# Kernel optimization log

Hardware: AMD Instinct MI355X
Metric: run time of the kernel (lower is better)

The kernel has to match this reference:

```python
import jax, jax.numpy as jnp
import numpy as np

B, N, D, R, W, H, I = 256, 2048, 128, 4, 1, 1024, 1024
CI = I + R * D                       # controller input size (1536)
IF = 2 * D * W + 2 * W + 1 + 4 * R + D * R   # interface size (787)
OPI = H + R * D                      # output_proj input (1536)


def _norm(v):
    # F.normalize(dim=-1): x / max(||x||, eps)
    return v / jnp.maximum(jnp.linalg.norm(v, axis=-1, keepdims=True), 1e-12)


def setup_inputs() -> dict:
    key = jax.random.key(0)
    ks = jax.random.split(key, 16)
    u = lambda k, shape, fan: jax.random.uniform(k, shape, jnp.float32, -1.0 / np.sqrt(fan), 1.0 / np.sqrt(fan))
    return {
        "x": jax.random.normal(ks[0], (B, I), jnp.float32),
        "memory": jax.random.normal(ks[1], (N, D), jnp.float32) * np.sqrt(2.0 / (N + D)),  # xavier-ish
        "usage": jax.random.uniform(ks[2], (N,), jnp.float32),          # usage in [0,1)
        "link": jax.random.normal(ks[3], (N, N), jnp.float32) * 0.01,   # non-trivial link state
        "W_ih": u(ks[4], (4 * H, CI), H),
        "W_hh": u(ks[5], (4 * H, H), H),
        "b_ih": u(ks[6], (4 * H,), H),
        "b_hh": u(ks[7], (4 * H,), H),
        "W_if": u(ks[8], (IF, H), H),
        "b_if": u(ks[9], (IF,), H),
        "W_out": u(ks[10], (H, OPI), OPI),
        "b_out": u(ks[11], (H,), OPI),
    }


def reference(x, memory, usage, link, W_ih, W_hh, b_ih, b_hh, W_if, b_if, W_out, b_out):
    # initial uniform read weights (prev state at first step)
    prev_rw = jnp.full((B, R, N), 1.0 / N, x.dtype)
    read_flat = (prev_rw @ memory).reshape(B, -1)                 # (B, R*D)
    cin = jnp.concatenate([x, read_flat], axis=-1)                # (B, CI)

    # single LSTM step, h0 = c0 = 0, torch gate order i,f,g,o
    g = cin @ W_ih.T + b_ih + b_hh
    gi, gf, gg, go = jnp.split(g, 4, axis=-1)
    c = jax.nn.sigmoid(gi) * jnp.tanh(gg)
    h = jax.nn.sigmoid(go) * jnp.tanh(c)                          # (B, H) controller out

    itf = h @ W_if.T + b_if                                       # (B, IF)
    o = 0
    write_vals = itf[:, o:o + D * W].reshape(B, W, D); o += D * W
    erase = jax.nn.sigmoid(itf[:, o:o + D * W]).reshape(B, W, D); o += D * W
    write_gates = jax.nn.sigmoid(itf[:, o:o + W]); o += W         # (B, W)
    alloc_gate = jax.nn.sigmoid(itf[:, o:o + 1]); o += 1          # (B, 1)
    o += W                                                        # free gates (parsed, unused)
    read_modes = jax.nn.softmax(itf[:, o:o + 3 * R].reshape(B, R, 3), -1); o += 3 * R
    read_str = jax.nn.softplus(itf[:, o:o + R]); o += R           # (B, R)
    read_keys = itf[:, o:o + D * R].reshape(B, R, D)

    # content addressing for the write (strength = 1)
    mem_n = _norm(memory)
    cw = jax.nn.softmax(_norm(write_vals.mean(1)) @ mem_n.T, -1)  # (B, N)

    # allocation weighting: sorted-usage cumprod (per source semantics)
    idx = jnp.argsort(usage)
    su = usage[idx]
    cp = jnp.cumprod(1.0 - su)
    alloc_s = jnp.concatenate([su[:1], su[1:] * cp[:-1]])
    alloc = jnp.zeros_like(usage).at[idx].set(alloc_s)[None, :] * alloc_gate  # (B, N)

    write_w = write_gates[:, :, None] * (0.5 * cw + 0.5 * alloc)[:, None, :]  # (B, W, N)

    # temporal link update: batch-mean of diag-masked outer product, decay 0.9
    lu = jnp.einsum('bwn,bwm->nm', write_w, write_w) / B
    lu = lu * (1.0 - jnp.eye(N, dtype=lu.dtype))
    link_new = link * 0.9 + lu * 0.1

    # memory write (erase then add, batch-mean)
    ev = erase * write_gates[:, :, None]
    av = write_vals * write_gates[:, :, None]
    erase_mat = jnp.einsum('bwn,bwd->nd', write_w, ev) / B
    add_mat = jnp.einsum('bwn,bwd->nd', write_w, av) / B
    mem_new = memory * (1.0 - erase_mat) + add_mat

    # read addressing on updated memory and updated link (all R heads vectorized)
    sim = jnp.einsum('brd,nd->brn', _norm(read_keys), _norm(mem_new))
    content_r = jax.nn.softmax(sim * read_str[:, :, None], -1)    # (B, R, N)
    backward_w = jnp.einsum('brn,nm->brm', prev_rw, link_new)     # mode 1: prev @ L
    forward_w = jnp.einsum('brn,mn->brm', prev_rw, link_new)      # mode 2: prev @ L^T
    new_rw = (read_modes[..., 0:1] * content_r
              + read_modes[..., 1:2] * backward_w
              + read_modes[..., 2:3] * forward_w)                 # (B, R, N)

    read_out = (new_rw @ mem_new).reshape(B, -1)                  # (B, R*D)
    out = jnp.concatenate([h, read_out], axis=-1) @ W_out.T + b_out
    return out
```

## Files before the change

### kernel.cpp

```cpp
#include <hip/hip_runtime.h>
#include <cmath>

#define DEVI __device__ __forceinline__

DEVI float sigm(float x){ return 1.f/(1.f+expf(-x)); }

typedef __attribute__((ext_vector_type(8))) _Float16 half8;
typedef __attribute__((ext_vector_type(4))) _Float16 half4;
typedef __attribute__((ext_vector_type(4))) float float4v;


__global__ void k_zero(float* __restrict__ p, int n){
  int i = blockIdx.x*256 + threadIdx.x;
  if (i < n) p[i] = 0.f;
}

__global__ __launch_bounds__(256) void k_stage1(
    const float* __restrict__ mem, float* __restrict__ cm, _Float16* __restrict__ mem_h,
    const float* __restrict__ usage, float* __restrict__ alloc,
    const float* __restrict__ link, float* __restrict__ rsl, float* __restrict__ cslp)
{
  __shared__ float smem[4][132];
  const int blk = blockIdx.x, t = threadIdx.x;
  const int wv = t >> 6, lane = t & 63;

  if (blk < 128){
    int rbase = blk*16 + wv*4;
    float x0[4], x1[4], ss[4];
    #pragma unroll
    for (int u = 0; u < 4; u++){
      const float* a = mem + (size_t)(rbase+u)*128;
      x0[u] = a[lane]; x1[u] = a[lane+64];
    }
    #pragma unroll
    for (int u = 0; u < 4; u++) ss[u] = x0[u]*x0[u] + x1[u]*x1[u];
    #pragma unroll
    for (int o = 1; o < 64; o <<= 1){
      #pragma unroll
      for (int u = 0; u < 4; u++) ss[u] += __shfl_xor(ss[u], o);
    }
    float c0 = 0.f, c1 = 0.f;
    #pragma unroll
    for (int u = 0; u < 4; u++){
      float invn = 1.f / fmaxf(sqrtf(ss[u]), 1e-12f);
      mem_h[(size_t)(rbase+u)*128 + lane]      = (_Float16)(x0[u]*invn);
      mem_h[(size_t)(rbase+u)*128 + 64 + lane] = (_Float16)(x1[u]*invn);
      c0 += x0[u]; c1 += x1[u];
    }
    smem[wv][lane] = c0; smem[wv][64+lane] = c1;
    __syncthreads();
    if (t < 128) atomicAdd(&cm[t], smem[0][t]+smem[1][t]+smem[2][t]+smem[3][t]);
  } else if (blk < 384){
    int pb = blk - 128;
    int r0 = pb*8;
    int c0 = t*8;
    float4v v0[8], v1[8];
    #pragma unroll
    for (int u = 0; u < 8; u++){
      const float* lp = link + (size_t)(r0+u)*2048 + c0;
      v0[u] = *(const float4v*)lp;
      v1[u] = *(const float4v*)(lp+4);
    }
    float colacc[8];
    #pragma unroll
    for (int j = 0; j < 8; j++) colacc[j] = 0.f;
    float rowpart[8];
    #pragma unroll
    for (int u = 0; u < 8; u++){
      float s = 0.f;
      #pragma unroll
      for (int j = 0; j < 4; j++){
        colacc[j]   += v0[u][j]; colacc[4+j] += v1[u][j];
        s += v0[u][j] + v1[u][j];
      }
      rowpart[u] = s;
    }
    #pragma unroll
    for (int o = 1; o < 64; o <<= 1){
      #pragma unroll
      for (int u = 0; u < 8; u++) rowpart[u] += __shfl_xor(rowpart[u], o);
    }
    if (lane == 0){
      #pragma unroll
      for (int u = 0; u < 8; u++) smem[wv][u] = rowpart[u];
    }
    __syncthreads();
    if (t < 8) rsl[r0+t] = smem[0][t]+smem[1][t]+smem[2][t]+smem[3][t];
    float4v w0, w1;
    #pragma unroll
    for (int j = 0; j < 4; j++){ w0[j] = colacc[j]; w1[j] = colacc[4+j]; }
    *(float4v*)&cslp[(size_t)pb*2048 + c0]     = w0;
    *(float4v*)&cslp[(size_t)pb*2048 + c0 + 4] = w1;
  } else {
    int n = (blk - 384)*4 + wv;
    float un = usage[n];
    float prod = 1.f;
    #pragma unroll
    for (int i = 0; i < 32; i++){
      int m = lane + i*64;
      float um = usage[m];
      bool before = (um < un) || (um == un && m < n);
      prod *= before ? (1.f - um) : 1.f;
    }
    #pragma unroll
    for (int o = 32; o > 0; o >>= 1) prod *= __shfl_xor(prod, o);
    if (lane == 0) alloc[n] = un * prod;
  }
}

__global__ __launch_bounds__(256) void k_cin_csl(const float* __restrict__ x,
    const float* __restrict__ cm, _Float16* __restrict__ cin,
    const float* __restrict__ cslp, float* __restrict__ csl)
{
  __shared__ float sm[4][64];
  int blk = blockIdx.x, t = threadIdx.x;
  if (blk < 1536){
    int idx = blk*256 + t;
    int b = idx / 1536, k = idx - b*1536;
    float v = (k < 1024) ? x[b*1024 + k] : cm[(k-1024) & 127] * (1.f/2048.f);
    cin[idx] = (_Float16)v;
  } else {
    int j = blk - 1536;
    int tl = t & 63, q = t >> 6;
    int col = j*64 + tl;
    float s = 0.f;
    for (int p = q*64; p < q*64 + 64; p += 4){
      s += cslp[(size_t)(p+0)*2048 + col] + cslp[(size_t)(p+1)*2048 + col]
         + cslp[(size_t)(p+2)*2048 + col] + cslp[(size_t)(p+3)*2048 + col];
    }
    sm[q][tl] = s;
    __syncthreads();
    if (q == 0) csl[col] = sm[0][tl]+sm[1][tl]+sm[2][tl]+sm[3][tl];
  }
}

#define QA 264
#define QB 520
#define QB3 776

template<typename TB> struct BReg;
template<> struct BReg<_Float16>{
  half8 v;
  DEVI void load(const _Float16* p){ v = *(const half8*)p; }
  DEVI half8 get() const { return v; }
};
template<> struct BReg<float>{
  float4v a, b;
  DEVI void load(const float* p){ a = *(const float4v*)p; b = *(const float4v*)(p+4); }
  DEVI half8 get() const {
    half8 h;
    #pragma unroll
    for (int j = 0; j < 4; j++){ h[j] = (_Float16)a[j]; h[4+j] = (_Float16)b[j]; }
    return h;
  }
};

template<typename TB>
__global__ __launch_bounds__(256) void gemm_t(
    const _Float16* __restrict__ A, const TB* __restrict__ Bm, float* __restrict__ C,
    int M, int N, int K,
    const float* __restrict__ bias1, const float* __restrict__ bias2)
{
  __shared__ _Float16 Ah[2][8*QA];
  __shared__ _Float16 Bh[2][8*QB];
  const int tid = threadIdx.x;
  const int m0 = blockIdx.y*32, n0 = blockIdx.x*64;
  const int T = K >> 6;
  const int arow = tid >> 3, aq = tid & 7;
  const int brow = tid >> 3, bq = tid & 7;
  int nB0 = n0 + brow;      if (nB0 >= N) nB0 = N - 1;
  int nB1 = n0 + brow + 32; if (nB1 >= N) nB1 = N - 1;
  const _Float16* Aptr = A + (size_t)(m0 + arow)*K + aq*8;
  const TB* Bp0 = Bm + (size_t)nB0*K + bq*8;
  const TB* Bp1 = Bm + (size_t)nB1*K + bq*8;
  const int wA  = aq*QA + arow*8;
  const int wB0 = bq*QB + brow*8;
  const int wB1 = bq*QB + (brow+32)*8;
  const int wv_ = tid >> 6, lane = tid & 63;
  const int fq = lane >> 4, fr = lane & 15;
  const int m16 = (wv_ & 1)*16, nb = (wv_ >> 1)*32;

  half8 ra;
  BReg<TB> rb0, rb1;
  ra = *(const half8*)(Aptr);
  rb0.load(Bp0);
  rb1.load(Bp1);
  *(half8*)&Ah[0][wA]  = ra;
  *(half8*)&Bh[0][wB0] = rb0.get();
  *(half8*)&Bh[0][wB1] = rb1.get();
  __syncthreads();

  float4v acc0 = {0.f,0.f,0.f,0.f}, acc1 = {0.f,0.f,0.f,0.f};
  for (int t = 0; t < T; t++){
    const int cur = t & 1, nxt = cur ^ 1;
    if (t+1 < T){
      ra = *(const half8*)(Aptr + (t+1)*64);
      rb0.load(Bp0 + (t+1)*64);
      rb1.load(Bp1 + (t+1)*64);
    }
    #pragma unroll
    for (int s = 0; s < 2; s++){
      int q = s*4 + fq;
      half8 a  = *(half8*)&Ah[cur][q*QA + (m16+fr)*8];
      half8 b0 = *(half8*)&Bh[cur][q*QB + (nb+fr)*8];
      half8 b1 = *(half8*)&Bh[cur][q*QB + (nb+16+fr)*8];
      acc0 = __builtin_amdgcn_mfma_f32_16x16x32_f16(a, b0, acc0, 0, 0, 0);
      acc1 = __builtin_amdgcn_mfma_f32_16x16x32_f16(a, b1, acc1, 0, 0, 0);
    }
    if (t+1 < T){
      *(half8*)&Ah[nxt][wA]  = ra;
      *(half8*)&Bh[nxt][wB0] = rb0.get();
      *(half8*)&Bh[nxt][wB1] = rb1.get();
    }
    __syncthreads();
  }

  const int colA = n0 + nb + fr, colB = colA + 16;
  #pragma unroll
  for (int i = 0; i < 4; i++){
    int m = m0 + m16 + fq*4 + i;
    if (colA < N){
      float v = acc0[i];
      if (bias1) v += bias1[colA];
      if (bias2) v += bias2[colA];
      C[(size_t)m*N + colA] = v;
    }
    if (colB < N){
      float v = acc1[i];
      if (bias1) v += bias1[colB];
      if (bias2) v += bias2[colB];
      C[(size_t)m*N + colB] = v;
    }
  }
}

__global__ __launch_bounds__(256) void k_gemm_lstm(
    const _Float16* __restrict__ A, const float* __restrict__ W,
    const float* __restrict__ b_ih, const float* __restrict__ b_hh,
    _Float16* __restrict__ h)
{
  __shared__ _Float16 Ah[2][8*QA];
  __shared__ _Float16 Bh[2][8*QB3];
  const int tid = threadIdx.x;
  const int m0 = blockIdx.y*32, c0 = blockIdx.x*32;
  const int T = 24;
  const int arow = tid >> 3, aq = tid & 7;
  const int brow = tid >> 3, bq = tid & 7;
  const _Float16* Aptr = A + (size_t)(m0 + arow)*1536 + aq*8;
  const float* Bpi = W + (size_t)(       c0 + brow)*1536 + bq*8;
  const float* Bpg = W + (size_t)(2048 + c0 + brow)*1536 + bq*8;
  const float* Bpo = W + (size_t)(3072 + c0 + brow)*1536 + bq*8;
  const int wA  = aq*QA + arow*8;
  const int wBi = bq*QB3 + brow*8;
  const int wBg = bq*QB3 + (32+brow)*8;
  const int wBo = bq*QB3 + (64+brow)*8;
  const int wv_ = tid >> 6, lane = tid & 63;
  const int fq = lane >> 4, fr = lane & 15;
  const int m16 = (wv_ & 1)*16, c16 = (wv_ >> 1)*16;

  half8 ra0, ra1;
  BReg<float> ri0, rg0, ro0, ri1, rg1, ro1;
  ra0 = *(const half8*)(Aptr);
  ri0.load(Bpi); rg0.load(Bpg); ro0.load(Bpo);
  ra1 = *(const half8*)(Aptr + 64);
  ri1.load(Bpi + 64); rg1.load(Bpg + 64); ro1.load(Bpo + 64);
  *(half8*)&Ah[0][wA]  = ra0;
  *(half8*)&Bh[0][wBi] = ri0.get();
  *(half8*)&Bh[0][wBg] = rg0.get();
  *(half8*)&Bh[0][wBo] = ro0.get();
  __syncthreads();

  float4v acci = {0.f,0.f,0.f,0.f}, accg = {0.f,0.f,0.f,0.f}, acco = {0.f,0.f,0.f,0.f};
  for (int t = 0; t < T; t++){
    const int cur = t & 1, nxt = cur ^ 1;
    if (t+2 < T){
      if (cur == 0){
        ra0 = *(const half8*)(Aptr + (t+2)*64);
        ri0.load(Bpi + (t+2)*64); rg0.load(Bpg + (t+2)*64); ro0.load(Bpo + (t+2)*64);
      } else {
        ra1 = *(const half8*)(Aptr + (t+2)*64);
        ri1.load(Bpi + (t+2)*64); rg1.load(Bpg + (t+2)*64); ro1.load(Bpo + (t+2)*64);
      }
    }
    #pragma unroll
    for (int s = 0; s < 2; s++){
      int q = s*4 + fq;
      half8 a  = *(half8*)&Ah[cur][q*QA + (m16+fr)*8];
      half8 bi = *(half8*)&Bh[cur][q*QB3 + (c16+fr)*8];
      half8 bg = *(half8*)&Bh[cur][q*QB3 + (32+c16+fr)*8];
      half8 bo = *(half8*)&Bh[cur][q*QB3 + (64+c16+fr)*8];
      acci = __builtin_amdgcn_mfma_f32_16x16x32_f16(a, bi, acci, 0, 0, 0);
      accg = __builtin_amdgcn_mfma_f32_16x16x32_f16(a, bg, accg, 0, 0, 0);
      acco = __builtin_amdgcn_mfma_f32_16x16x32_f16(a, bo, acco, 0, 0, 0);
    }
    if (t+1 < T){
      if (nxt == 1){
        *(half8*)&Ah[1][wA]  = ra1;
        *(half8*)&Bh[1][wBi] = ri1.get();
        *(half8*)&Bh[1][wBg] = rg1.get();
        *(half8*)&Bh[1][wBo] = ro1.get();
      } else {
        *(half8*)&Ah[0][wA]  = ra0;
        *(half8*)&Bh[0][wBi] = ri0.get();
        *(half8*)&Bh[0][wBg] = rg0.get();
        *(half8*)&Bh[0][wBo] = ro0.get();
      }
    }
    __syncthreads();
  }

  const int col = c0 + c16 + fr;
  const float bi1 = b_ih[col]        + b_hh[col];
  const float bg1 = b_ih[2048 + col] + b_hh[2048 + col];
  const float bo1 = b_ih[3072 + col] + b_hh[3072 + col];
  #pragma unroll
  for (int i = 0; i < 4; i++){
    int m = m0 + m16 + fq*4 + i;
    float gi = acci[i] + bi1;
    float gg = accg[i] + bg1;
    float go = acco[i] + bo1;
    float c = sigm(gi) * tanhf(gg);
    h[(size_t)m*1024 + col] = (_Float16)(sigm(go) * tanhf(c));
  }
}

DEVI float blockReduce128(float v, float* lds2){
  #pragma unroll
  for (int o = 32; o > 0; o >>= 1) v += __shfl_xor(v, o);
  int w = threadIdx.x >> 6;
  __syncthreads();
  if ((threadIdx.x & 63) == 0) lds2[w] = v;
  __syncthreads();
  return lds2[0] + lds2[1];
}

__global__ __launch_bounds__(128) void k_parse(const float* __restrict__ itf,
    _Float16* __restrict__ wv_h, float* __restrict__ ev, float* __restrict__ av,
    float* __restrict__ wg_, float* __restrict__ ag_,
    float* __restrict__ rm0, float* __restrict__ rm1, float* __restrict__ rm2,
    _Float16* __restrict__ rks_h)
{
  __shared__ float red[2];
  int b = blockIdx.x, t = threadIdx.x;
  const float* it = itf + (size_t)b*787;
  float wg = sigm(it[256]);
  float ag = sigm(it[257]);
  if (t == 0){ wg_[b] = wg; ag_[b] = ag; }
  float w = it[t];
  av[b*128 + t] = w * wg;
  ev[b*128 + t] = sigm(it[128 + t]) * wg;
  float ss = blockReduce128(w*w, red);
  float invwv = 1.f / fmaxf(sqrtf(ss), 1e-12f);
  wv_h[b*128 + t] = (_Float16)(w * invwv);
  if (t < 4){
    int rr = t;
    float m0v = it[259 + rr*3 + 0], m1v = it[259 + rr*3 + 1], m2v = it[259 + rr*3 + 2];
    float mx = fmaxf(m0v, fmaxf(m1v, m2v));
    float e0 = expf(m0v - mx), e1 = expf(m1v - mx), e2 = expf(m2v - mx);
    float inv = 1.f / (e0 + e1 + e2);
    rm0[b*4 + rr] = e0*inv; rm1[b*4 + rr] = e1*inv; rm2[b*4 + rr] = e2*inv;
  }
  #pragma unroll
  for (int rr = 0; rr < 4; rr++){
    float kv = it[275 + rr*128 + t];
    float ks = blockReduce128(kv*kv, red);
    float sx = it[271 + rr];
    float str = fmaxf(sx, 0.f) + log1pf(expf(-fabsf(sx)));
    float invk = 1.f / fmaxf(sqrtf(ks), 1e-12f);
    rks_h[((size_t)b*4 + rr)*128 + t] = (_Float16)(kv * invk * str);
  }
}

__global__ __launch_bounds__(256) void k_softmax_ww(float* __restrict__ P,
    const float* __restrict__ alloc, const float* __restrict__ wg, const float* __restrict__ ag){
  __shared__ float red[4];
  float* p = P + (size_t)blockIdx.x*2048;
  int t = threadIdx.x;
  float r[8];
  float mx = -3.4e38f;
  #pragma unroll
  for (int i = 0; i < 8; i++){ r[i] = p[t + i*256]; mx = fmaxf(mx, r[i]); }
  #pragma unroll
  for (int o = 32; o > 0; o >>= 1) mx = fmaxf(mx, __shfl_xor(mx, o));
  if ((t & 63) == 0) red[t >> 6] = mx;
  __syncthreads();
  mx = fmaxf(fmaxf(red[0], red[1]), fmaxf(red[2], red[3]));
  float s = 0.f;
  #pragma unroll
  for (int i = 0; i < 8; i++){ r[i] = expf(r[i] - mx); s += r[i]; }
  #pragma unroll
  for (int o = 32; o > 0; o >>= 1) s += __shfl_xor(s, o);
  __syncthreads();
  if ((t & 63) == 0) red[t >> 6] = s;
  __syncthreads();
  s = red[0] + red[1] + red[2] + red[3];
  float inv = 1.f / s;
  float wgb = wg[blockIdx.x], agb = ag[blockIdx.x];
  #pragma unroll
  for (int i = 0; i < 8; i++){
    int col = t + i*256;
    p[col] = wgb*(0.5f*r[i]*inv + 0.5f*alloc[col]*agb);
  }
}

__global__ __launch_bounds__(256) void k_memupdate_fused(const float* __restrict__ ww,
    const float* __restrict__ ev, const float* __restrict__ av,
    const float* __restrict__ mem,
    const float* __restrict__ wg, const float* __restrict__ ag,
    const float* __restrict__ alloc,
    const float* __restrict__ rsl, const float* __restrict__ csl,
    _Float16* __restrict__ memn_h, _Float16* __restrict__ memnT_h,
    float* __restrict__ bwm, float* __restrict__ fwm)
{
  __shared__ float Ws[16][34];
  __shared__ float Es[16][132], Vs[16][132];
  __shared__ float lb[128], lf[128];
  __shared__ _Float16 Traw[32][132];
  __shared__ float tbs[256];
  __shared__ float sq[8][32], sd[8][32];
  __shared__ float bwL[32], fwL[32];
  __shared__ float sred[4];
  const int n0 = blockIdx.x*32;
  const int tid = threadIdx.x, tx = tid & 31, ty = tid >> 5;

  {
    float sa = 0.f;
    #pragma unroll
    for (int i = 0; i < 8; i++) sa += alloc[tid + i*256];
    #pragma unroll
    for (int o = 32; o > 0; o >>= 1) sa += __shfl_xor(sa, o);
    if ((tid & 63) == 0) sred[tid >> 6] = sa;
    if (tid < 128){ lb[tid] = 0.f; lf[tid] = 0.f; }
    __syncthreads();
    sa = (sred[0]+sred[1]) + (sred[2]+sred[3]);
    tbs[tid] = wg[tid]*(0.5f + 0.5f*ag[tid]*sa);
  }

  const int wk = tid >> 4, wn = (tid & 15)*2;
  const int ek = tid >> 4, ec = (tid & 15)*8;
  float ae[4][4] = {}, aa[4][4] = {};
  float qp = 0.f, ddp = 0.f;
  for (int k0 = 0; k0 < 256; k0 += 16){
    float2 vw  = *(const float2*)(ww + (size_t)(k0+wk)*2048 + n0 + wn);
    float4 ve0 = *(const float4*)(ev + (size_t)(k0+ek)*128 + ec);
    float4 ve1 = *(const float4*)(ev + (size_t)(k0+ek)*128 + ec + 4);
    float4 va0 = *(const float4*)(av + (size_t)(k0+ek)*128 + ec);
    float4 va1 = *(const float4*)(av + (size_t)(k0+ek)*128 + ec + 4);
    __syncthreads();
    Ws[wk][wn] = vw.x; Ws[wk][wn+1] = vw.y;
    *(float4*)&Es[ek][ec] = ve0; *(float4*)&Es[ek][ec+4] = ve1;
    *(float4*)&Vs[ek][ec] = va0; *(float4*)&Vs[ek][ec+4] = va1;
    __syncthreads();
    #pragma unroll
    for (int k = 0; k < 16; k++){
      float a[4], e[4], v[4];
      #pragma unroll
      for (int i = 0; i < 4; i++) a[i] = Ws[k][ty*4+i];
      #pragma unroll
      for (int j = 0; j < 4; j++){ e[j] = Es[k][tx*4+j]; v[j] = Vs[k][tx*4+j]; }
      #pragma unroll
      for (int i = 0; i < 4; i++)
        #pragma unroll
        for (int j = 0; j < 4; j++){
          ae[i][j] = fmaf(a[i], e[j], ae[i][j]);
          aa[i][j] = fmaf(a[i], v[j], aa[i][j]);
        }
    }
    {
      float w0 = Ws[ty*2+0][tx], w1 = Ws[ty*2+1][tx];
      qp  = fmaf(tbs[k0+ty*2+0], w0, qp);  ddp = fmaf(w0, w0, ddp);
      qp  = fmaf(tbs[k0+ty*2+1], w1, qp);  ddp = fmaf(w1, w1, ddp);
    }
  }
  sq[ty][tx] = qp; sd[ty][tx] = ddp;
  __syncthreads();
  if (tid < 32){
    float q = 0.f, dd = 0.f;
    #pragma unroll
    for (int z = 0; z < 8; z++){ q += sq[z][tid]; dd += sd[z][tid]; }
    float lus = (q - dd) * (1.f/256.f);
    bwL[tid] = (0.9f*csl[n0+tid] + 0.1f*lus) * (1.f/2048.f);
    fwL[tid] = (0.9f*rsl[n0+tid] + 0.1f*lus) * (1.f/2048.f);
  }
  __syncthreads();

  float ab[4] = {0,0,0,0}, af[4] = {0,0,0,0};
  #pragma unroll
  for (int i = 0; i < 4; i++){
    int n = n0 + ty*4 + i;
    float bwn = bwL[ty*4+i], fwn = fwL[ty*4+i];
    float v[4]; float ss = 0.f;
    #pragma unroll
    for (int j = 0; j < 4; j++){
      int d = tx*4 + j;
      float em = ae[i][j]*(1.f/256.f), am = aa[i][j]*(1.f/256.f);
      float mv = mem[(size_t)n*128 + d]*(1.f - em) + am;
      v[j] = mv; ss += mv*mv;
      ab[j] = fmaf(bwn, mv, ab[j]);
      af[j] = fmaf(fwn, mv, af[j]);
    }
    #pragma unroll
    for (int o = 1; o < 32; o <<= 1) ss += __shfl_xor(ss, o);
    float invn = 1.f / fmaxf(sqrtf(ss), 1e-12f);
    half4 hn, hr;
    #pragma unroll
    for (int j = 0; j < 4; j++){ hn[j] = (_Float16)(v[j]*invn); hr[j] = (_Float16)v[j]; }
    *(half4*)(memn_h + (size_t)n*128 + tx*4) = hn;
    *(half4*)&Traw[ty*4+i][tx*4] = hr;
  }
  __syncthreads();
  {
    int d = tid >> 1, seg = (tid & 1)*16;
    half8 o0, o1;
    #pragma unroll
    for (int j = 0; j < 8; j++){ o0[j] = Traw[seg+j][d]; o1[j] = Traw[seg+8+j][d]; }
    *(half8*)(memnT_h + (size_t)d*2048 + n0 + seg)     = o0;
    *(half8*)(memnT_h + (size_t)d*2048 + n0 + seg + 8) = o1;
  }
  #pragma unroll
  for (int j = 0; j < 4; j++){
    atomicAdd(&lb[tx*4+j], ab[j]);
    atomicAdd(&lf[tx*4+j], af[j]);
  }
  __syncthreads();
  if (tid < 128){
    atomicAdd(&bwm[tid], lb[tid]);
    atomicAdd(&fwm[tid], lf[tid]);
  }
}

__global__ __launch_bounds__(256) void k_flash(
    const _Float16* __restrict__ Q, const _Float16* __restrict__ Kh,
    const _Float16* __restrict__ Vt,
    float* __restrict__ pacc, float* __restrict__ pm, float* __restrict__ pl)
{
  __shared__ _Float16 Pl[4][16][32];
  __shared__ float cmb[4][2080];
  __shared__ float scl[4][16];
  const int tid = threadIdx.x;
  const int qt = blockIdx.x >> 2, kc = blockIdx.x & 3;
  const int wv = tid >> 6, lane = tid & 63;
  const int fq = lane >> 4, fr = lane & 15;
  const int kw0 = kc*512 + wv*128;

  half8 aq[4];
  #pragma unroll
  for (int c = 0; c < 4; c++)
    aq[c] = *(const half8*)(Q + (size_t)(qt*16 + fr)*128 + c*32 + fq*8);

  float m[4] = {-3.0e38f,-3.0e38f,-3.0e38f,-3.0e38f};
  float l[4] = {0.f,0.f,0.f,0.f};
  float4v acc[8] = {};
  for (int s = 0; s < 4; s++){
    const int kb = kw0 + s*32;
    float4v S0 = {0,0,0,0}, S1 = {0,0,0,0};
    #pragma unroll
    for (int c = 0; c < 4; c++){
      half8 b0 = *(const half8*)(Kh + (size_t)(kb + fr)*128      + c*32 + fq*8);
      half8 b1 = *(const half8*)(Kh + (size_t)(kb + 16 + fr)*128 + c*32 + fq*8);
      S0 = __builtin_amdgcn_mfma_f32_16x16x32_f16(aq[c], b0, S0, 0, 0, 0);
      S1 = __builtin_amdgcn_mfma_f32_16x16x32_f16(aq[c], b1, S1, 0, 0, 0);
    }
    float mt[4], ps[4];
    #pragma unroll
    for (int i = 0; i < 4; i++) mt[i] = fmaxf(S0[i], S1[i]);
    #pragma unroll
    for (int o = 1; o < 16; o <<= 1){
      #pragma unroll
      for (int i = 0; i < 4; i++) mt[i] = fmaxf(mt[i], __shfl_xor(mt[i], o));
    }
    #pragma unroll
    for (int i = 0; i < 4; i++){
      float mn = fmaxf(m[i], mt[i]);
      float al = expf(m[i] - mn);
      float p0 = expf(S0[i] - mn), p1 = expf(S1[i] - mn);
      S0[i] = p0; S1[i] = p1;
      ps[i] = p0 + p1;
      l[i] *= al;
      m[i] = mn;
      #pragma unroll
      for (int c = 0; c < 8; c++) acc[c][i] *= al;
    }
    #pragma unroll
    for (int o = 1; o < 16; o <<= 1){
      #pragma unroll
      for (int i = 0; i < 4; i++) ps[i] += __shfl_xor(ps[i], o);
    }
    #pragma unroll
    for (int i = 0; i < 4; i++) l[i] += ps[i];
    #pragma unroll
    for (int i = 0; i < 4; i++){
      Pl[wv][fq*4+i][fr]      = (_Float16)S0[i];
      Pl[wv][fq*4+i][16 + fr] = (_Float16)S1[i];
    }
    half8 pf = *(half8*)&Pl[wv][fr][fq*8];
    #pragma unroll
    for (int c = 0; c < 8; c++){
      half8 bv = *(const half8*)(Vt + (size_t)(c*16 + fr)*2048 + kb + fq*8);
      acc[c] = __builtin_amdgcn_mfma_f32_16x16x32_f16(pf, bv, acc[c], 0, 0, 0);
    }
  }
  if (fr == 0){
    #pragma unroll
    for (int i = 0; i < 4; i++){
      cmb[wv][fq*4+i]      = m[i];
      cmb[wv][16 + fq*4+i] = l[i];
    }
  }
  #pragma unroll
  for (int c = 0; c < 8; c++)
    #pragma unroll
    for (int i = 0; i < 4; i++)
      cmb[wv][32 + (fq*4+i)*128 + c*16 + fr] = acc[c][i];
  __syncthreads();
  if (tid < 16){
    float mm = fmaxf(fmaxf(cmb[0][tid], cmb[1][tid]), fmaxf(cmb[2][tid], cmb[3][tid]));
    float ll = 0.f;
    #pragma unroll
    for (int w = 0; w < 4; w++){
      float e = expf(cmb[w][tid] - mm);
      scl[w][tid] = e;
      ll += e * cmb[w][16 + tid];
    }
    pm[blockIdx.x*16 + tid] = mm;
    pl[blockIdx.x*16 + tid] = ll;
  }
  __syncthreads();
  for (int e = tid; e < 2048; e += 256){
    int q = e >> 7;
    float a = scl[0][q]*cmb[0][32+e] + scl[1][q]*cmb[1][32+e]
            + scl[2][q]*cmb[2][32+e] + scl[3][q]*cmb[3][32+e];
    pacc[(size_t)blockIdx.x*2048 + e] = a;
  }
}

__global__ void k_hro_comb(const _Float16* __restrict__ h, const float* __restrict__ pacc,
                           const float* __restrict__ pm, const float* __restrict__ pl,
                           const float* __restrict__ rm0, const float* __restrict__ rm1,
                           const float* __restrict__ rm2, const float* __restrict__ bwm,
                           const float* __restrict__ fwm, _Float16* __restrict__ hro){
  int idx = blockIdx.x*256 + threadIdx.x;
  int b = idx / 1536, k = idx - b*1536;
  if (k < 1024){
    hro[idx] = h[b*1024 + k];
  } else {
    int r = k - 1024, rh = r >> 7, d = r & 127;
    int row = b*4 + rh, qt = row >> 4, q = row & 15;
    float mm = -3.0e38f;
    #pragma unroll
    for (int kc = 0; kc < 4; kc++) mm = fmaxf(mm, pm[(qt*4+kc)*16 + q]);
    float num = 0.f, den = 0.f;
    #pragma unroll
    for (int kc = 0; kc < 4; kc++){
      float e = expf(pm[(qt*4+kc)*16 + q] - mm);
      den += e * pl[(qt*4+kc)*16 + q];
      num += e * pacc[(size_t)(qt*4+kc)*2048 + q*128 + d];
    }
    float pv = num / den;
    hro[idx] = (_Float16)(rm0[row]*pv + rm1[row]*bwm[d] + rm2[row]*fwm[d]);
  }
}


extern "C" void kernel_launch(void* const* d_in, const int* in_sizes, int n_in,
                              void* d_out, int out_size, void* d_ws, size_t ws_size,
                              hipStream_t stream)
{
  const float* x     = (const float*)d_in[0];
  const float* mem   = (const float*)d_in[1];
  const float* usage = (const float*)d_in[2];
  const float* link  = (const float*)d_in[3];
  const float* W_ih  = (const float*)d_in[4];
  const float* b_ih  = (const float*)d_in[6];
  const float* b_hh  = (const float*)d_in[7];
  const float* W_if  = (const float*)d_in[8];
  const float* b_if  = (const float*)d_in[9];
  const float* W_out = (const float*)d_in[10];
  const float* b_out = (const float*)d_in[11];
  float* out = (float*)d_out;
  float* ws  = (float*)d_ws;

  float* cm     = ws + 0;
  float* csl    = ws + 128;
  float* bwm    = ws + 2176;
  float* fwm    = ws + 2304;
  float* wg     = ws + 6784;
  float* ag     = ws + 7040;
  float* rm0    = ws + 7296;
  float* rm1    = ws + 8320;
  float* rm2    = ws + 9344;
  float* alloc  = ws + 10368;
  float* rsl    = ws + 12416;
  float* ev     = ws + 14464;
  float* av     = ws + 47232;
  float* itf    = ws + 1128576;
  float* ww     = ws + 1330048;
  float* pacc   = ws + 1854336;
  float* pm     = ws + 2378624;
  float* pl     = ws + 2382720;
  _Float16* wv_h    = (_Float16*)(ws + 2386816);
  _Float16* mem_h   = (_Float16*)(ws + 2403200);
  _Float16* memn_h  = (_Float16*)(ws + 2534272);
  _Float16* memnT_h = (_Float16*)(ws + 2665344);
  _Float16* rks_h   = (_Float16*)(ws + 2796416);
  _Float16* hro_h   = (_Float16*)(ws + 2861952);
  _Float16* cin_h   = (_Float16*)(ws + 3058560);
  _Float16* h_h     = (_Float16*)(ws + 3255168);
  float* cslp       = ws + 3386240;

  k_zero<<<10, 256, 0, stream>>>(ws, 2432);

  k_stage1<<<896, 256, 0, stream>>>(mem, cm, mem_h, usage, alloc, link, rsl, cslp);
  k_cin_csl<<<1568, 256, 0, stream>>>(x, cm, cin_h, cslp, csl);

  k_gemm_lstm<<<dim3(32,8), 256, 0, stream>>>(cin_h, W_ih, b_ih, b_hh, h_h);

  gemm_t<float><<<dim3(13,8), 256, 0, stream>>>(h_h, W_if, itf, 256, 787, 1024, b_if, nullptr);
  k_parse<<<256, 128, 0, stream>>>(itf, wv_h, ev, av, wg, ag, rm0, rm1, rm2, rks_h);

  gemm_t<_Float16><<<dim3(32,8), 256, 0, stream>>>(wv_h, mem_h, ww, 256, 2048, 128, nullptr, nullptr);
  k_softmax_ww<<<256, 256, 0, stream>>>(ww, alloc, wg, ag);

  k_memupdate_fused<<<64, 256, 0, stream>>>(ww, ev, av, mem, wg, ag, alloc, rsl, csl,
                                            memn_h, memnT_h, bwm, fwm);

  k_flash<<<256, 256, 0, stream>>>(rks_h, memn_h, memnT_h, pacc, pm, pl);

  k_hro_comb<<<1536, 256, 0, stream>>>(h_h, pacc, pm, pl, rm0, rm1, rm2, bwm, fwm, hro_h);
  gemm_t<float><<<dim3(16,8), 256, 0, stream>>>(hro_h, W_out, out, 256, 1024, 1536, b_out, nullptr);

  (void)in_sizes; (void)n_in; (void)out_size; (void)ws_size;
}
```

Baseline: 238.1 us.

## Fuse cin build into LSTM GEMM, softmax into write GEMM, csl into memupdate

Removes the k_cin_csl kernel by having the LSTM GEMM read x and the mean-read vector directly and convert them to fp16 while loading tiles. It also folds the column-sum reduction of the link partials into the memory-update kernel. The write-weight softmax kernel is replaced by an exp epilogue in the write GEMM that atomically accumulates row sums, with normalization and the allocation mix applied when the memory-update kernel loads the tiles. This drops two launches and a round trip over the 256x2048 matrix, but the exp has no max subtraction (overflow risk if logits grow large) and the atomics make the row sums nondeterministic.

```diff
diff --git a/kernel.cpp b/kernel.cpp
--- a/kernel.cpp
+++ b/kernel.cpp
@@ -105,32 +105,6 @@
     #pragma unroll
     for (int o = 32; o > 0; o >>= 1) prod *= __shfl_xor(prod, o);
     if (lane == 0) alloc[n] = un * prod;
-  }
-}
-
-__global__ __launch_bounds__(256) void k_cin_csl(const float* __restrict__ x,
-    const float* __restrict__ cm, _Float16* __restrict__ cin,
-    const float* __restrict__ cslp, float* __restrict__ csl)
-{
-  __shared__ float sm[4][64];
-  int blk = blockIdx.x, t = threadIdx.x;
-  if (blk < 1536){
-    int idx = blk*256 + t;
-    int b = idx / 1536, k = idx - b*1536;
-    float v = (k < 1024) ? x[b*1024 + k] : cm[(k-1024) & 127] * (1.f/2048.f);
-    cin[idx] = (_Float16)v;
-  } else {
-    int j = blk - 1536;
-    int tl = t & 63, q = t >> 6;
-    int col = j*64 + tl;
-    float s = 0.f;
-    for (int p = q*64; p < q*64 + 64; p += 4){
-      s += cslp[(size_t)(p+0)*2048 + col] + cslp[(size_t)(p+1)*2048 + col]
-         + cslp[(size_t)(p+2)*2048 + col] + cslp[(size_t)(p+3)*2048 + col];
-    }
-    sm[q][tl] = s;
-    __syncthreads();
-    if (q == 0) csl[col] = sm[0][tl]+sm[1][tl]+sm[2][tl]+sm[3][tl];
   }
 }
 
@@ -151,6 +125,22 @@
     half8 h;
     #pragma unroll
     for (int j = 0; j < 4; j++){ h[j] = (_Float16)a[j]; h[4+j] = (_Float16)b[j]; }
+    return h;
+  }
+};
+
+struct ARegX {
+  float4v a, b; float sc;
+  DEVI void load(const float* __restrict__ x, const float* __restrict__ cm, int row, int k){
+    const float* p;
+    if (k < 1024){ p = x + (size_t)row*1024 + k; sc = 1.f; }
+    else         { p = cm + ((k - 1024) & 127); sc = (1.f/2048.f); }
+    a = *(const float4v*)p; b = *(const float4v*)(p+4);
+  }
+  DEVI half8 get() const {
+    half8 h;
+    #pragma unroll
+    for (int j = 0; j < 4; j++){ h[j] = (_Float16)(a[j]*sc); h[4+j] = (_Float16)(b[j]*sc); }
     return h;
   }
 };
@@ -234,8 +224,77 @@
   }
 }
 
+__global__ __launch_bounds__(256) void k_gemm_wwExp(
+    const _Float16* __restrict__ A, const _Float16* __restrict__ Bm,
+    float* __restrict__ C, float* __restrict__ rsum)
+{
+  __shared__ _Float16 Ah[2][8*QA];
+  __shared__ _Float16 Bh[2][8*QB];
+  const int tid = threadIdx.x;
+  const int m0 = blockIdx.y*32, n0 = blockIdx.x*64;
+  const int arow = tid >> 3, aq = tid & 7;
+  const int brow = tid >> 3, bq = tid & 7;
+  const _Float16* Aptr = A + (size_t)(m0 + arow)*128 + aq*8;
+  const _Float16* Bp0 = Bm + (size_t)(n0 + brow)*128 + bq*8;
+  const _Float16* Bp1 = Bm + (size_t)(n0 + brow + 32)*128 + bq*8;
+  const int wA  = aq*QA + arow*8;
+  const int wB0 = bq*QB + brow*8;
+  const int wB1 = bq*QB + (brow+32)*8;
+  const int wv_ = tid >> 6, lane = tid & 63;
+  const int fq = lane >> 4, fr = lane & 15;
+  const int m16 = (wv_ & 1)*16, nb = (wv_ >> 1)*32;
+
+  half8 ra  = *(const half8*)(Aptr);
+  half8 rb0 = *(const half8*)(Bp0);
+  half8 rb1 = *(const half8*)(Bp1);
+  *(half8*)&Ah[0][wA]  = ra;
+  *(half8*)&Bh[0][wB0] = rb0;
+  *(half8*)&Bh[0][wB1] = rb1;
+  __syncthreads();
+
+  float4v acc0 = {0.f,0.f,0.f,0.f}, acc1 = {0.f,0.f,0.f,0.f};
+  for (int t = 0; t < 2; t++){
+    const int cur = t & 1, nxt = cur ^ 1;
+    if (t == 0){
+      ra  = *(const half8*)(Aptr + 64);
+      rb0 = *(const half8*)(Bp0 + 64);
+      rb1 = *(const half8*)(Bp1 + 64);
+    }
+    #pragma unroll
+    for (int s = 0; s < 2; s++){
+      int q = s*4 + fq;
+      half8 a  = *(half8*)&Ah[cur][q*QA + (m16+fr)*8];
+      half8 b0 = *(half8*)&Bh[cur][q*QB + (nb+fr)*8];
+      half8 b1 = *(half8*)&Bh[cur][q*QB + (nb+16+fr)*8];
+      acc0 = __builtin_amdgcn_mfma_f32_16x16x32_f16(a, b0, acc0, 0, 0, 0);
+      acc1 = __builtin_amdgcn_mfma_f32_16x16x32_f16(a, b1, acc1, 0, 0, 0);
+    }
+    if (t == 0){
+      *(half8*)&Ah[nxt][wA]  = ra;
+      *(half8*)&Bh[nxt][wB0] = rb0;
+      *(half8*)&Bh[nxt][wB1] = rb1;
+    }
+    __syncthreads();
+  }
+
+  const int colA = n0 + nb + fr, colB = colA + 16;
+  #pragma unroll
+  for (int i = 0; i < 4; i++){
+    int m = m0 + m16 + fq*4 + i;
+    float e0 = expf(acc0[i]);
+    float e1 = expf(acc1[i]);
+    C[(size_t)m*2048 + colA] = e0;
+    C[(size_t)m*2048 + colB] = e1;
+    float rs = e0 + e1;
+    #pragma unroll
+    for (int o = 1; o < 16; o <<= 1) rs += __shfl_xor(rs, o);
+    if (fr == 0) atomicAdd(&rsum[m], rs);
+  }
+}
+
 __global__ __launch_bounds__(256) void k_gemm_lstm(
-    const _Float16* __restrict__ A, const float* __restrict__ W,
+    const float* __restrict__ x, const float* __restrict__ cm,
+    const float* __restrict__ W,
     const float* __restrict__ b_ih, const float* __restrict__ b_hh,
     _Float16* __restrict__ h)
 {
@@ -246,7 +305,7 @@
   const int T = 24;
   const int arow = tid >> 3, aq = tid & 7;
   const int brow = tid >> 3, bq = tid & 7;
-  const _Float16* Aptr = A + (size_t)(m0 + arow)*1536 + aq*8;
+  const int arw = m0 + arow;
   const float* Bpi = W + (size_t)(       c0 + brow)*1536 + bq*8;
   const float* Bpg = W + (size_t)(2048 + c0 + brow)*1536 + bq*8;
   const float* Bpo = W + (size_t)(3072 + c0 + brow)*1536 + bq*8;
@@ -258,13 +317,13 @@
   const int fq = lane >> 4, fr = lane & 15;
   const int m16 = (wv_ & 1)*16, c16 = (wv_ >> 1)*16;
 
-  half8 ra0, ra1;
+  ARegX ax0, ax1;
   BReg<float> ri0, rg0, ro0, ri1, rg1, ro1;
-  ra0 = *(const half8*)(Aptr);
+  ax0.load(x, cm, arw, aq*8);
   ri0.load(Bpi); rg0.load(Bpg); ro0.load(Bpo);
-  ra1 = *(const half8*)(Aptr + 64);
+  ax1.load(x, cm, arw, aq*8 + 64);
   ri1.load(Bpi + 64); rg1.load(Bpg + 64); ro1.load(Bpo + 64);
-  *(half8*)&Ah[0][wA]  = ra0;
+  *(half8*)&Ah[0][wA]  = ax0.get();
   *(half8*)&Bh[0][wBi] = ri0.get();
   *(half8*)&Bh[0][wBg] = rg0.get();
   *(half8*)&Bh[0][wBo] = ro0.get();
@@ -275,10 +334,10 @@
     const int cur = t & 1, nxt = cur ^ 1;
     if (t+2 < T){
       if (cur == 0){
-        ra0 = *(const half8*)(Aptr + (t+2)*64);
+        ax0.load(x, cm, arw, aq*8 + (t+2)*64);
         ri0.load(Bpi + (t+2)*64); rg0.load(Bpg + (t+2)*64); ro0.load(Bpo + (t+2)*64);
       } else {
-        ra1 = *(const half8*)(Aptr + (t+2)*64);
+        ax1.load(x, cm, arw, aq*8 + (t+2)*64);
         ri1.load(Bpi + (t+2)*64); rg1.load(Bpg + (t+2)*64); ro1.load(Bpo + (t+2)*64);
       }
     }
@@ -295,12 +354,12 @@
     }
     if (t+1 < T){
       if (nxt == 1){
-        *(half8*)&Ah[1][wA]  = ra1;
+        *(half8*)&Ah[1][wA]  = ax1.get();
         *(half8*)&Bh[1][wBi] = ri1.get();
         *(half8*)&Bh[1][wBg] = rg1.get();
         *(half8*)&Bh[1][wBo] = ro1.get();
       } else {
-        *(half8*)&Ah[0][wA]  = ra0;
+        *(half8*)&Ah[0][wA]  = ax0.get();
         *(half8*)&Bh[0][wBi] = ri0.get();
         *(half8*)&Bh[0][wBg] = rg0.get();
         *(half8*)&Bh[0][wBo] = ro0.get();
@@ -371,44 +430,12 @@
   }
 }
 
-__global__ __launch_bounds__(256) void k_softmax_ww(float* __restrict__ P,
-    const float* __restrict__ alloc, const float* __restrict__ wg, const float* __restrict__ ag){
-  __shared__ float red[4];
-  float* p = P + (size_t)blockIdx.x*2048;
-  int t = threadIdx.x;
-  float r[8];
-  float mx = -3.4e38f;
-  #pragma unroll
-  for (int i = 0; i < 8; i++){ r[i] = p[t + i*256]; mx = fmaxf(mx, r[i]); }
-  #pragma unroll
-  for (int o = 32; o > 0; o >>= 1) mx = fmaxf(mx, __shfl_xor(mx, o));
-  if ((t & 63) == 0) red[t >> 6] = mx;
-  __syncthreads();
-  mx = fmaxf(fmaxf(red[0], red[1]), fmaxf(red[2], red[3]));
-  float s = 0.f;
-  #pragma unroll
-  for (int i = 0; i < 8; i++){ r[i] = expf(r[i] - mx); s += r[i]; }
-  #pragma unroll
-  for (int o = 32; o > 0; o >>= 1) s += __shfl_xor(s, o);
-  __syncthreads();
-  if ((t & 63) == 0) red[t >> 6] = s;
-  __syncthreads();
-  s = red[0] + red[1] + red[2] + red[3];
-  float inv = 1.f / s;
-  float wgb = wg[blockIdx.x], agb = ag[blockIdx.x];
-  #pragma unroll
-  for (int i = 0; i < 8; i++){
-    int col = t + i*256;
-    p[col] = wgb*(0.5f*r[i]*inv + 0.5f*alloc[col]*agb);
-  }
-}
-
 __global__ __launch_bounds__(256) void k_memupdate_fused(const float* __restrict__ ww,
     const float* __restrict__ ev, const float* __restrict__ av,
     const float* __restrict__ mem,
     const float* __restrict__ wg, const float* __restrict__ ag,
-    const float* __restrict__ alloc,
-    const float* __restrict__ rsl, const float* __restrict__ csl,
+    const float* __restrict__ alloc, const float* __restrict__ rsum,
+    const float* __restrict__ rsl, const float* __restrict__ cslp,
     _Float16* __restrict__ memn_h, _Float16* __restrict__ memnT_h,
     float* __restrict__ bwm, float* __restrict__ fwm)
 {
@@ -416,8 +443,10 @@
   __shared__ float Es[16][132], Vs[16][132];
   __shared__ float lb[128], lf[128];
   __shared__ _Float16 Traw[32][132];
-  __shared__ float tbs[256];
+  __shared__ float tbs[256], c1s[256], c2s[256];
+  __shared__ float allocL[32];
   __shared__ float sq[8][32], sd[8][32];
+  __shared__ float cpart[8][32];
   __shared__ float bwL[32], fwL[32];
   __shared__ float sred[4];
   const int n0 = blockIdx.x*32;
@@ -431,10 +460,24 @@
     for (int o = 32; o > 0; o >>= 1) sa += __shfl_xor(sa, o);
     if ((tid & 63) == 0) sred[tid >> 6] = sa;
     if (tid < 128){ lb[tid] = 0.f; lf[tid] = 0.f; }
+    if (tid < 32) allocL[tid] = alloc[n0 + tid];
     __syncthreads();
     sa = (sred[0]+sred[1]) + (sred[2]+sred[3]);
-    tbs[tid] = wg[tid]*(0.5f + 0.5f*ag[tid]*sa);
-  }
+    float w = wg[tid], a = ag[tid];
+    tbs[tid] = w*(0.5f + 0.5f*a*sa);
+    c1s[tid] = 0.5f*w / rsum[tid];
+    c2s[tid] = 0.5f*w*a;
+  }
+  {
+    int col = n0 + tx;
+    float s = 0.f;
+    for (int p = ty*32; p < ty*32 + 32; p += 4){
+      s += cslp[(size_t)(p+0)*2048 + col] + cslp[(size_t)(p+1)*2048 + col]
+         + cslp[(size_t)(p+2)*2048 + col] + cslp[(size_t)(p+3)*2048 + col];
+    }
+    cpart[ty][tx] = s;
+  }
+  __syncthreads();
 
   const int wk = tid >> 4, wn = (tid & 15)*2;
   const int ek = tid >> 4, ec = (tid & 15)*8;
@@ -447,7 +490,11 @@
     float4 va0 = *(const float4*)(av + (size_t)(k0+ek)*128 + ec);
     float4 va1 = *(const float4*)(av + (size_t)(k0+ek)*128 + ec + 4);
     __syncthreads();
-    Ws[wk][wn] = vw.x; Ws[wk][wn+1] = vw.y;
+    {
+      float cb1 = c1s[k0+wk], cb2 = c2s[k0+wk];
+      Ws[wk][wn]   = cb1*vw.x + cb2*allocL[wn];
+      Ws[wk][wn+1] = cb1*vw.y + cb2*allocL[wn+1];
+    }
     *(float4*)&Es[ek][ec] = ve0; *(float4*)&Es[ek][ec+4] = ve1;
     *(float4*)&Vs[ek][ec] = va0; *(float4*)&Vs[ek][ec+4] = va1;
     __syncthreads();
@@ -475,11 +522,11 @@
   sq[ty][tx] = qp; sd[ty][tx] = ddp;
   __syncthreads();
   if (tid < 32){
-    float q = 0.f, dd = 0.f;
-    #pragma unroll
-    for (int z = 0; z < 8; z++){ q += sq[z][tid]; dd += sd[z][tid]; }
+    float q = 0.f, dd = 0.f, cs = 0.f;
+    #pragma unroll
+    for (int z = 0; z < 8; z++){ q += sq[z][tid]; dd += sd[z][tid]; cs += cpart[z][tid]; }
     float lus = (q - dd) * (1.f/256.f);
-    bwL[tid] = (0.9f*csl[n0+tid] + 0.1f*lus) * (1.f/2048.f);
+    bwL[tid] = (0.9f*cs + 0.1f*lus) * (1.f/2048.f);
     fwL[tid] = (0.9f*rsl[n0+tid] + 0.1f*lus) * (1.f/2048.f);
   }
   __syncthreads();
@@ -681,9 +728,9 @@
   float* ws  = (float*)d_ws;
 
   float* cm     = ws + 0;
-  float* csl    = ws + 128;
   float* bwm    = ws + 2176;
   float* fwm    = ws + 2304;
+  float* rsum   = ws + 2432;
   float* wg     = ws + 6784;
   float* ag     = ws + 7040;
   float* rm0    = ws + 7296;
@@ -704,25 +751,22 @@
   _Float16* memnT_h = (_Float16*)(ws + 2665344);
   _Float16* rks_h   = (_Float16*)(ws + 2796416);
   _Float16* hro_h   = (_Float16*)(ws + 2861952);
-  _Float16* cin_h   = (_Float16*)(ws + 3058560);
   _Float16* h_h     = (_Float16*)(ws + 3255168);
   float* cslp       = ws + 3386240;
 
-  k_zero<<<10, 256, 0, stream>>>(ws, 2432);
+  k_zero<<<11, 256, 0, stream>>>(ws, 2688);
 
   k_stage1<<<896, 256, 0, stream>>>(mem, cm, mem_h, usage, alloc, link, rsl, cslp);
-  k_cin_csl<<<1568, 256, 0, stream>>>(x, cm, cin_h, cslp, csl);
-
-  k_gemm_lstm<<<dim3(32,8), 256, 0, stream>>>(cin_h, W_ih, b_ih, b_hh, h_h);
+
+  k_gemm_lstm<<<dim3(32,8), 256, 0, stream>>>(x, cm, W_ih, b_ih, b_hh, h_h);
 
   gemm_t<float><<<dim3(13,8), 256, 0, stream>>>(h_h, W_if, itf, 256, 787, 1024, b_if, nullptr);
   k_parse<<<256, 128, 0, stream>>>(itf, wv_h, ev, av, wg, ag, rm0, rm1, rm2, rks_h);
 
-  gemm_t<_Float16><<<dim3(32,8), 256, 0, stream>>>(wv_h, mem_h, ww, 256, 2048, 128, nullptr, nullptr);
-  k_softmax_ww<<<256, 256, 0, stream>>>(ww, alloc, wg, ag);
-
-  k_memupdate_fused<<<64, 256, 0, stream>>>(ww, ev, av, mem, wg, ag, alloc, rsl, csl,
-                                            memn_h, memnT_h, bwm, fwm);
+  k_gemm_wwExp<<<dim3(32,8), 256, 0, stream>>>(wv_h, mem_h, ww, rsum);
+
+  k_memupdate_fused<<<64, 256, 0, stream>>>(ww, ev, av, mem, wg, ag, alloc, rsum,
+                                            rsl, cslp, memn_h, memnT_h, bwm, fwm);
 
   k_flash<<<256, 256, 0, stream>>>(rks_h, memn_h, memnT_h, pacc, pm, pl);
 
```

New measurement: 233.8 us. About the same (-1.8%).
